# Optimization experiments

Hardware: AMD Instinct MI355X
Metric: run time of the kernel (lower is better)

## Reference

```python
import jax, jax.numpy as jnp
import numpy as np

H, W = 1024, 1024
K = 15            # degree_max / neighbour_nb
GAMMA = 0.5
MULTIPLIER = 1.0
WIN = 4           # half window for neighbor offsets (window_size=9)


def setup_inputs() -> dict:
    key = jax.random.key(0)
    k1, k2, k3, k4, k5 = jax.random.split(key, 5)
    N = H * W
    sig1 = jax.random.normal(k1, (1, 1, H, W), dtype=jnp.float32)
    sig2 = jax.random.normal(k2, (1, 2, H, W), dtype=jnp.float32)
    weights = jax.random.uniform(k3, (K, N), dtype=jnp.float32)
    # Build a local-window neighbor graph, as similarity_graph would produce.
    idx = jnp.arange(N, dtype=jnp.int32)
    y = idx // W
    x = idx % W
    dy = jax.random.randint(k4, (K, N), -WIN, WIN + 1, dtype=jnp.int32)
    dx = jax.random.randint(k5, (K, N), -WIN, WIN + 1, dtype=jnp.int32)
    yn = jnp.clip(y[None] + dy, 0, H - 1)
    xn = jnp.clip(x[None] + dx, 0, W - 1)
    neighbours = (yn * W + xn).astype(jnp.int32)            # (K, N)
    # dist = (x_source - x_target, y_source - y_target), per constructor.
    dist = jnp.stack([(x[None] - xn), (y[None] - yn)], axis=1).astype(jnp.float32)  # (K, 2, N)
    return {"sig1": sig1, "sig2": sig2, "weights": weights, "dist": dist,
            "neighbours": neighbours}


def reference(sig1, sig2, weights, dist, neighbours):
    N = weights.shape[1]
    s1 = sig1.reshape(-1)                 # (N,)
    s2 = sig2.reshape(2, -1)              # (2, N)
    # planar term: sum_c sig2[c, n] * dist[k, c, n]  -> (K, N)
    plane = jnp.einsum('cn,kcn->kn', s2, dist)
    aux1 = s1[None, :] - s1[neighbours] - plane           # (K, N)
    aux1 = jnp.sqrt(jnp.sum((aux1 * weights) ** 2, axis=0)).sum()
    # vector-field difference: (K, 2, N), norm over channel dim
    diff2 = s2[None, :, :] - jnp.transpose(s2[:, neighbours], (1, 0, 2))
    aux2 = jnp.sqrt(jnp.sum(diff2 * diff2, axis=1))        # (K, N)
    aux2 = jnp.sum(aux2 * weights)
    loss = (aux1 + GAMMA * aux2) / N
    return MULTIPLIER * loss
```

## Files before the change

kernel.cpp:

```cpp
#include <hip/hip_runtime.h>
#include <hip/hip_bf16.h>

#define HH 1024
#define WW 1024
#define NN (HH * WW)
#define KK 15
#define GAMMA_F 0.5f

__global__ __launch_bounds__(256) void ppr_kernel(
    const float* __restrict__ s1,
    const float* __restrict__ s2,
    const float* __restrict__ w,
    const float* __restrict__ dist,
    const int* __restrict__ nb,
    float* __restrict__ out)
{
    const int n = blockIdx.x * blockDim.x + threadIdx.x;

    int   j[KK];
    float wk[KK], d0[KK], d1[KK];
#pragma unroll
    for (int k = 0; k < KK; ++k) j[k]  = nb[(size_t)k * NN + n];
#pragma unroll
    for (int k = 0; k < KK; ++k) wk[k] = w[(size_t)k * NN + n];
#pragma unroll
    for (int k = 0; k < KK; ++k) {
        d0[k] = dist[(size_t)(2 * k + 0) * NN + n];
        d1[k] = dist[(size_t)(2 * k + 1) * NN + n];
    }

    const float s1n = s1[n];
    const float s2a = s2[n];
    const float s2b = s2[NN + n];

    float g1[KK], g2a[KK], g2b[KK];
#pragma unroll
    for (int k = 0; k < KK; ++k) g1[k]  = s1[j[k]];
#pragma unroll
    for (int k = 0; k < KK; ++k) g2a[k] = s2[j[k]];
#pragma unroll
    for (int k = 0; k < KK; ++k) g2b[k] = s2[NN + j[k]];

    float acc1 = 0.0f, acc2 = 0.0f;
#pragma unroll
    for (int k = 0; k < KK; ++k) {
        const float plane = fmaf(s2a, d0[k], s2b * d1[k]);
        const float a1 = (s1n - g1[k] - plane) * wk[k];
        acc1 = fmaf(a1, a1, acc1);

        const float e0 = s2a - g2a[k];
        const float e1 = s2b - g2b[k];
        acc2 = fmaf(sqrtf(fmaf(e0, e0, e1 * e1)), wk[k], acc2);
    }
    float local = sqrtf(acc1) + GAMMA_F * acc2;

#pragma unroll
    for (int off = 32; off > 0; off >>= 1)
        local += __shfl_down(local, off, 64);

    __shared__ float smem[4];
    const int wave = threadIdx.x >> 6;
    const int lane = threadIdx.x & 63;
    if (lane == 0) smem[wave] = local;
    __syncthreads();

    if (threadIdx.x == 0) {
        const float s = smem[0] + smem[1] + smem[2] + smem[3];
        atomicAdd(out, s * (1.0f / (float)NN));
    }
}

extern "C" void kernel_launch(void* const* d_in, const int* in_sizes, int n_in,
                              void* d_out, int out_size, void* d_ws, size_t ws_size,
                              hipStream_t stream) {
    const float* s1   = (const float*)d_in[0];
    const float* s2   = (const float*)d_in[1];
    const float* w    = (const float*)d_in[2];
    const float* dist = (const float*)d_in[3];
    const int*   nb   = (const int*)d_in[4];
    float* out = (float*)d_out;

    hipMemsetAsync(out, 0, sizeof(float) * (size_t)out_size, stream);

    const int block = 256;
    const int grid  = NN / block;
    ppr_kernel<<<grid, block, 0, stream>>>(s1, s2, w, dist, nb, out);
}
```

Before: 298.3 us.

## Stage 9-row halo tile of s1/s2 in LDS for neighbour gathers

Each block first cooperatively loads a 9-row by 264-column halo tile of s1 and both s2 channels into shared memory. The 45 per-thread neighbour gathers then read from LDS instead of issuing scattered global loads. This relies on every neighbour lying within the ±4 row/column window around its point, which holds for the input construction but not for arbitrary graphs. The tile takes about 28 KB of LDS per block, which may limit occupancy, and the halo rows are reloaded redundantly across blocks.

After: 286.5 us. 1.04x faster.

```diff
diff --git a/kernel.cpp b/kernel.cpp
--- a/kernel.cpp
+++ b/kernel.cpp
@@ -7,6 +7,9 @@
 #define KK 15
 #define GAMMA_F 0.5f
 
+#define TROWS 9
+#define TW    264
+
 __global__ __launch_bounds__(256) void ppr_kernel(
     const float* __restrict__ s1,
     const float* __restrict__ s2,
@@ -15,7 +18,37 @@
     const int* __restrict__ nb,
     float* __restrict__ out)
 {
-    const int n = blockIdx.x * blockDim.x + threadIdx.x;
+    __shared__ float ls1[TROWS * TW];
+    __shared__ float l2a[TROWS * TW];
+    __shared__ float l2b[TROWS * TW];
+
+    const int tid = threadIdx.x;
+    const int n   = blockIdx.x * 256 + tid;
+    const int y   = n >> 10;
+    const int c0  = (blockIdx.x & 3) << 8;
+
+#pragma unroll
+    for (int r = 0; r < TROWS; ++r) {
+        int gy = y - 4 + r;
+        gy = gy < 0 ? 0 : (gy > HH - 1 ? HH - 1 : gy);
+        const float* ps1 = s1 + (size_t)gy * WW;
+        const float* p2a = s2 + (size_t)gy * WW;
+        const float* p2b = s2 + NN + (size_t)gy * WW;
+
+        int gx = c0 - 4 + tid;
+        gx = gx < 0 ? 0 : (gx > WW - 1 ? WW - 1 : gx);
+        ls1[r * TW + tid] = ps1[gx];
+        l2a[r * TW + tid] = p2a[gx];
+        l2b[r * TW + tid] = p2b[gx];
+        if (tid < TW - 256) {
+            int gx2 = c0 - 4 + 256 + tid;
+            gx2 = gx2 > WW - 1 ? WW - 1 : gx2;
+            ls1[r * TW + 256 + tid] = ps1[gx2];
+            l2a[r * TW + 256 + tid] = p2a[gx2];
+            l2b[r * TW + 256 + tid] = p2b[gx2];
+        }
+    }
+    __syncthreads();
 
     int   j[KK];
     float wk[KK], d0[KK], d1[KK];
@@ -29,42 +62,43 @@
         d1[k] = dist[(size_t)(2 * k + 1) * NN + n];
     }
 
-    const float s1n = s1[n];
-    const float s2a = s2[n];
-    const float s2b = s2[NN + n];
+    const int own = 4 * TW + tid + 4;
+    const float s1n = ls1[own];
+    const float s2a = l2a[own];
+    const float s2b = l2b[own];
 
-    float g1[KK], g2a[KK], g2b[KK];
-#pragma unroll
-    for (int k = 0; k < KK; ++k) g1[k]  = s1[j[k]];
-#pragma unroll
-    for (int k = 0; k < KK; ++k) g2a[k] = s2[j[k]];
-#pragma unroll
-    for (int k = 0; k < KK; ++k) g2b[k] = s2[NN + j[k]];
+    const int base = (4 - y) * TW + (4 - c0);
 
     float acc1 = 0.0f, acc2 = 0.0f;
 #pragma unroll
     for (int k = 0; k < KK; ++k) {
+        const int jj  = j[k];
+        const int off = (jj >> 10) * TW + (jj & (WW - 1)) + base;
+        const float g1  = ls1[off];
+        const float g2a = l2a[off];
+        const float g2b = l2b[off];
+
         const float plane = fmaf(s2a, d0[k], s2b * d1[k]);
-        const float a1 = (s1n - g1[k] - plane) * wk[k];
+        const float a1 = (s1n - g1 - plane) * wk[k];
         acc1 = fmaf(a1, a1, acc1);
 
-        const float e0 = s2a - g2a[k];
-        const float e1 = s2b - g2b[k];
+        const float e0 = s2a - g2a;
+        const float e1 = s2b - g2b;
         acc2 = fmaf(sqrtf(fmaf(e0, e0, e1 * e1)), wk[k], acc2);
     }
     float local = sqrtf(acc1) + GAMMA_F * acc2;
 
 #pragma unroll
-    for (int off = 32; off > 0; off >>= 1)
-        local += __shfl_down(local, off, 64);
+    for (int off2 = 32; off2 > 0; off2 >>= 1)
+        local += __shfl_down(local, off2, 64);
 
     __shared__ float smem[4];
-    const int wave = threadIdx.x >> 6;
-    const int lane = threadIdx.x & 63;
+    const int wave = tid >> 6;
+    const int lane = tid & 63;
     if (lane == 0) smem[wave] = local;
     __syncthreads();
 
-    if (threadIdx.x == 0) {
+    if (tid == 0) {
         const float s = smem[0] + smem[1] + smem[2] + smem[3];
         atomicAdd(out, s * (1.0f / (float)NN));
     }
```
